# Optimization experiments

Measured on AMD Instinct MI355X. Metric: run time of the kernel, lower is better.

The kernel has to match this reference:

```python
import jax, jax.numpy as jnp
import numpy as np

BATCH = 8
N_POINTS = 2048
HOP = 1  # hop_length


def setup_inputs() -> dict:
    key = jax.random.key(0)
    kx = jax.random.fold_in(key, 0)
    x = jax.random.normal(kx, (BATCH, N_POINTS), dtype=jnp.float32)
    # learnable window-width parameter (init_lambd = 20.0)
    lambd = jnp.full((1,), 20.0, dtype=jnp.float32)
    return {"x": x, "lambd": lambd}


def reference(x, lambd):
    """Batched differentiable Gaussian-window spectrogram.

    Equivalent to looping over the batch and calling
    tf.differentiable_spectrogram(x[i] - mean(x[i]), |lambd|, hop_length=HOP):
    a Gaussian window over the WHOLE signal centered at t_c = 0, HOP, ..., n,
    followed by a zero-padded one-sided FFT (n_fft = 2n) and power spectrum.
    Output: (B, 1, n+1, n//HOP + 1).
    """
    B, n = x.shape
    sigma = jnp.abs(lambd)[0]
    # per-sample mean subtraction
    x = x - jnp.mean(x, axis=1, keepdims=True)
    t = jnp.arange(n, dtype=jnp.float32)                       # (n,)
    t_c = jnp.arange(0, n + 1, HOP, dtype=jnp.float32)         # (F,) frame centers
    # Gaussian windows over the whole signal, one per frame center: (F, n)
    windows = jnp.exp(-0.5 * jnp.square((t[None, :] - t_c[:, None]) / sigma))
    # windowed signals: (B, F, n)
    xw = x[:, None, :] * windows[None, :, :]
    # zero-padded one-sided FFT -> n+1 frequency bins: (B, F, n+1)
    spec = jnp.fft.rfft(xw, n=2 * n, axis=-1)
    power = spec.real ** 2 + spec.imag ** 2                    # power spectrogram
    # (B, 1, n+1 freq, F time)
    return jnp.swapaxes(power, 1, 2)[:, None, :, :]
```

## Files before the change

kernel.cpp:

```cpp
#include <hip/hip_runtime.h>
#include <math.h>

#define NPTS    2048
#define NBINS   2049
#define NFRAMES 2049
#define U       192
#define PAD     96
#define XPLEN   2560

#define MTOT    4224
#define MBLK    33
#define NBLK    9
#define BM      128
#define BN      256
#define BK      64
#define SPAN    (BN + U)
#define SSTRIDE 464
#define NCOPY   8
#define ASTRIDE 72
#define ABUF    (BM * ASTRIDE)

typedef __attribute__((ext_vector_type(8))) short short8_t;
typedef __attribute__((ext_vector_type(4))) float float4_t;

static __device__ __forceinline__ unsigned short f2bf(float f) {
    unsigned u = __float_as_uint(f);
    unsigned r = (u + 0x7fffu + ((u >> 16) & 1u)) >> 16;
    return (unsigned short)r;
}

#define WCH 6
#define WGBLK ((MTOT * WCH + 255) / 256)
__global__ void prep_kernel(const float* __restrict__ x, const float* __restrict__ lambd,
                            unsigned short* __restrict__ xp, unsigned short* __restrict__ W) {
    if (blockIdx.x < 8) {
        __shared__ float red[256];
        const int b = blockIdx.x;
        float s = 0.f;
        for (int t = threadIdx.x; t < NPTS; t += 256) s += x[b * NPTS + t];
        red[threadIdx.x] = s;
        __syncthreads();
        for (int off = 128; off > 0; off >>= 1) {
            if (threadIdx.x < off) red[threadIdx.x] += red[threadIdx.x + off];
            __syncthreads();
        }
        const float mean = red[0] * (1.f / (float)NPTS);
        for (int t = threadIdx.x; t < XPLEN; t += 256) {
            const int s2 = t - PAD;
            float v = (s2 >= 0 && s2 < NPTS) ? (x[b * NPTS + s2] - mean) : 0.f;
            xp[b * XPLEN + t] = f2bf(v);
        }
        return;
    }
    const int idx = (blockIdx.x - 8) * 256 + threadIdx.x;
    if (idx >= MTOT * WCH) return;
    const int m  = idx / WCH;
    const int ch = idx - m * WCH;
    const int k = m >> 1, p = m & 1;
    unsigned int* wp = (unsigned int*)(W + (size_t)m * U + ch * 32);
    if (k >= NBINS) {
        #pragma unroll
        for (int j = 0; j < 16; ++j) wp[j] = 0u;
        return;
    }
    const float sigma  = fabsf(lambd[0]);
    const float inv2s2 = 0.5f / (sigma * sigma);
    const int   u0i = ch * 32 - PAD;
    const float u0  = (float)u0i;
    const float TWO_PI = 6.28318530717958647692f;
    float sn, cs, sd, cd;
    __sincosf(TWO_PI * (1.f / 4096.f) * (float)((k * u0i) & 4095), &sn, &cs);
    __sincosf(TWO_PI * (1.f / 4096.f) * (float)k, &sd, &cd);
    float       g  = __expf(-u0 * u0 * inv2s2);
    float       gr = __expf(-(2.f * u0 + 1.f) * inv2s2);
    const float gq = __expf(-2.f * inv2s2);
    #pragma unroll
    for (int j = 0; j < 16; ++j) {
        unsigned short lo = f2bf(g * (p ? sn : cs));
        float cn = cs * cd - sn * sd; sn = fmaf(sn, cd, cs * sd); cs = cn;
        g *= gr; gr *= gq;
        unsigned short hi = f2bf(g * (p ? sn : cs));
        cn = cs * cd - sn * sd; sn = fmaf(sn, cd, cs * sd); cs = cn;
        g *= gr; gr *= gq;
        wp[j] = (unsigned int)lo | ((unsigned int)hi << 16);
    }
}

__global__ __launch_bounds__(256, 2) void spec_mfma(
        const unsigned short* __restrict__ W, const unsigned short* __restrict__ xp,
        float* __restrict__ out) {
    __shared__ unsigned short Alds[2 * ABUF];
    __shared__ unsigned short span[NCOPY * SSTRIDE];

    const int tid = threadIdx.x;
    const int b  = blockIdx.z;
    const int n0 = blockIdx.x * BN;
    const int m0 = blockIdx.y * BM;

    {
        const unsigned short* xpb = xp + b * XPLEN;
        for (int i = tid; i < NCOPY * SPAN; i += 256) {
            const int c = i / SPAN;
            const int t = i - c * SPAN;
            span[c * SSTRIDE + t] = xpb[n0 + t + c];
        }
    }

    const int lane = tid & 63;
    const int wv   = tid >> 6;
    const int wm   = (wv & 1) * 64;
    const int wn   = (wv >> 1) * 128;
    const int col  = lane & 15;
    const int q    = lane >> 4;

    const int row  = tid >> 1;
    const int half = tid & 1;
    const unsigned short* wrow = W + (size_t)(m0 + row) * U + half * 32;
    const int lbase = row * ASTRIDE + half * 32;

    const int cc = col & 7;
    const unsigned short* bbase = span + cc * SSTRIDE + (wn + col - cc) + 8 * q;

    float4_t acc[4][8];
    #pragma unroll
    for (int mt = 0; mt < 4; ++mt)
        #pragma unroll
        for (int nt = 0; nt < 8; ++nt)
            acc[mt][nt] = (float4_t){0.f, 0.f, 0.f, 0.f};

    float4 r0, r1, r2, r3;
    {
        const float4* g4 = (const float4*)(wrow);
        r0 = g4[0]; r1 = g4[1]; r2 = g4[2]; r3 = g4[3];
        float4* l4 = (float4*)(Alds + lbase);
        l4[0] = r0; l4[1] = r1; l4[2] = r2; l4[3] = r3;
        const float4* g5 = (const float4*)(wrow + BK);
        r0 = g5[0]; r1 = g5[1]; r2 = g5[2]; r3 = g5[3];
    }
    __syncthreads();

    short8_t bf[8];
    #pragma unroll
    for (int d = 0; d < 8; ++d)
        bf[d] = *(const short8_t*)(bbase + 16 * d);

    #pragma unroll
    for (int s = 0; s < 3; ++s) {
        if (s < 2) {
            float4* l4 = (float4*)(Alds + ((s + 1) & 1) * ABUF + lbase);
            l4[0] = r0; l4[1] = r1; l4[2] = r2; l4[3] = r3;
        }
        if (s < 1) {
            const float4* g4 = (const float4*)(wrow + (s + 2) * BK);
            r0 = g4[0]; r1 = g4[1]; r2 = g4[2]; r3 = g4[3];
        }
        const unsigned short* cur = Alds + (s & 1) * ABUF;
        #pragma unroll
        for (int ks = 0; ks < 2; ++ks) {
            const int j  = s * 2 + ks;
            const int kk = ks * 32;
            short8_t af[4];
            #pragma unroll
            for (int mt = 0; mt < 4; ++mt)
                af[mt] = *(const short8_t*)(cur + (wm + mt * 16 + col) * ASTRIDE + kk + q * 8);
            short8_t nb0, nb1;
            if (j < 5) {
                nb0 = *(const short8_t*)(bbase + 16 * (2 * j + 8));
                nb1 = *(const short8_t*)(bbase + 16 * (2 * j + 9));
            }
            #pragma unroll
            for (int mt = 0; mt < 4; ++mt)
                #pragma unroll
                for (int nt = 0; nt < 8; ++nt)
                    acc[mt][nt] = __builtin_amdgcn_mfma_f32_16x16x32_bf16(
                        af[mt], bf[(nt + 2 * j) & 7], acc[mt][nt], 0, 0, 0);
            if (j < 5) {
                bf[(2 * j) & 7]     = nb0;
                bf[(2 * j + 1) & 7] = nb1;
            }
        }
        __syncthreads();
    }

    const int fbase = n0 + wn + col;
    #pragma unroll
    for (int mt = 0; mt < 4; ++mt) {
        const int mrow = m0 + wm + mt * 16 + q * 4;
        const int kk0  = mrow >> 1;
        #pragma unroll
        for (int nt = 0; nt < 8; ++nt) {
            const int f = fbase + nt * 16;
            if (f < NFRAMES) {
                const float4_t a = acc[mt][nt];
                const float p0 = a[0] * a[0] + a[1] * a[1];
                const float p1 = a[2] * a[2] + a[3] * a[3];
                if (kk0 < NBINS)
                    out[((size_t)b * NBINS + kk0) * NFRAMES + f] = p0;
                if (kk0 + 1 < NBINS)
                    out[((size_t)b * NBINS + kk0 + 1) * NFRAMES + f] = p1;
            }
        }
    }
}

extern "C" void kernel_launch(void* const* d_in, const int* in_sizes, int n_in,
                              void* d_out, int out_size, void* d_ws, size_t ws_size,
                              hipStream_t stream) {
    const float* x     = (const float*)d_in[0];
    const float* lambd = (const float*)d_in[1];
    float*       out   = (float*)d_out;

    char* ws = (char*)d_ws;
    unsigned short* xp = (unsigned short*)ws;
    unsigned short* W  = (unsigned short*)(ws + 43264);

    hipLaunchKernelGGL(prep_kernel, dim3(8 + WGBLK), dim3(256), 0, stream, x, lambd, xp, W);

    dim3 grid(NBLK, MBLK, 8);
    hipLaunchKernelGGL(spec_mfma, grid, dim3(256), 0, stream, W, xp, out);
}
```

Before: 172.1 us.

## Load A operand fragments directly from global memory, drop LDS staging

The W (A-operand) tiles are now read straight from global/L2 into registers in the MFMA fragment layout, with one-step register double buffering. This replaces the LDS double-buffered staging, removing LDS writes, LDS reads and the per-stage barriers. The span fill also writes two bf16 values per 32-bit store. The trade-off is uncoalesced 16-byte global loads per lane, and two waves sharing the same rows both fetch A, so more L2 traffic and global latency now sit on the MFMA critical path.

Result: slower. 176.0 us (+2.3%).

```diff
diff --git a/kernel.cpp b/kernel.cpp
--- a/kernel.cpp
+++ b/kernel.cpp
@@ -13,12 +13,9 @@
 #define NBLK    9
 #define BM      128
 #define BN      256
-#define BK      64
 #define SPAN    (BN + U)
 #define SSTRIDE 464
 #define NCOPY   8
-#define ASTRIDE 72
-#define ABUF    (BM * ASTRIDE)
 
 typedef __attribute__((ext_vector_type(8))) short short8_t;
 typedef __attribute__((ext_vector_type(4))) float float4_t;
@@ -89,7 +86,6 @@
 __global__ __launch_bounds__(256, 2) void spec_mfma(
         const unsigned short* __restrict__ W, const unsigned short* __restrict__ xp,
         float* __restrict__ out) {
-    __shared__ unsigned short Alds[2 * ABUF];
     __shared__ unsigned short span[NCOPY * SSTRIDE];
 
     const int tid = threadIdx.x;
@@ -99,10 +95,12 @@
 
     {
         const unsigned short* xpb = xp + b * XPLEN;
-        for (int i = tid; i < NCOPY * SPAN; i += 256) {
-            const int c = i / SPAN;
-            const int t = i - c * SPAN;
-            span[c * SSTRIDE + t] = xpb[n0 + t + c];
+        for (int i = tid; i < NCOPY * (SPAN / 2); i += 256) {
+            const int c  = i / (SPAN / 2);
+            const int t2 = (i - c * (SPAN / 2)) * 2;
+            const unsigned lo = xpb[n0 + t2 + c];
+            const unsigned hi = xpb[n0 + t2 + c + 1];
+            *(unsigned*)(span + c * SSTRIDE + t2) = lo | (hi << 16);
         }
     }
 
@@ -113,10 +111,7 @@
     const int col  = lane & 15;
     const int q    = lane >> 4;
 
-    const int row  = tid >> 1;
-    const int half = tid & 1;
-    const unsigned short* wrow = W + (size_t)(m0 + row) * U + half * 32;
-    const int lbase = row * ASTRIDE + half * 32;
+    const unsigned short* abase = W + (size_t)(m0 + wm + col) * U + q * 8;
 
     const int cc = col & 7;
     const unsigned short* bbase = span + cc * SSTRIDE + (wn + col - cc) + 8 * q;
@@ -128,15 +123,11 @@
         for (int nt = 0; nt < 8; ++nt)
             acc[mt][nt] = (float4_t){0.f, 0.f, 0.f, 0.f};
 
-    float4 r0, r1, r2, r3;
-    {
-        const float4* g4 = (const float4*)(wrow);
-        r0 = g4[0]; r1 = g4[1]; r2 = g4[2]; r3 = g4[3];
-        float4* l4 = (float4*)(Alds + lbase);
-        l4[0] = r0; l4[1] = r1; l4[2] = r2; l4[3] = r3;
-        const float4* g5 = (const float4*)(wrow + BK);
-        r0 = g5[0]; r1 = g5[1]; r2 = g5[2]; r3 = g5[3];
-    }
+    short8_t afc[4], afn[4];
+    #pragma unroll
+    for (int mt = 0; mt < 4; ++mt)
+        afc[mt] = *(const short8_t*)(abase + mt * 16 * U);
+
     __syncthreads();
 
     short8_t bf[8];
@@ -145,41 +136,28 @@
         bf[d] = *(const short8_t*)(bbase + 16 * d);
 
     #pragma unroll
-    for (int s = 0; s < 3; ++s) {
-        if (s < 2) {
-            float4* l4 = (float4*)(Alds + ((s + 1) & 1) * ABUF + lbase);
-            l4[0] = r0; l4[1] = r1; l4[2] = r2; l4[3] = r3;
-        }
-        if (s < 1) {
-            const float4* g4 = (const float4*)(wrow + (s + 2) * BK);
-            r0 = g4[0]; r1 = g4[1]; r2 = g4[2]; r3 = g4[3];
-        }
-        const unsigned short* cur = Alds + (s & 1) * ABUF;
-        #pragma unroll
-        for (int ks = 0; ks < 2; ++ks) {
-            const int j  = s * 2 + ks;
-            const int kk = ks * 32;
-            short8_t af[4];
+    for (int j = 0; j < 6; ++j) {
+        short8_t nb0, nb1;
+        if (j < 5) {
             #pragma unroll
             for (int mt = 0; mt < 4; ++mt)
-                af[mt] = *(const short8_t*)(cur + (wm + mt * 16 + col) * ASTRIDE + kk + q * 8);
-            short8_t nb0, nb1;
-            if (j < 5) {
-                nb0 = *(const short8_t*)(bbase + 16 * (2 * j + 8));
-                nb1 = *(const short8_t*)(bbase + 16 * (2 * j + 9));
-            }
+                afn[mt] = *(const short8_t*)(abase + mt * 16 * U + (j + 1) * 32);
+            nb0 = *(const short8_t*)(bbase + 16 * (2 * j + 8));
+            nb1 = *(const short8_t*)(bbase + 16 * (2 * j + 9));
+        }
+        #pragma unroll
+        for (int mt = 0; mt < 4; ++mt)
+            #pragma unroll
+            for (int nt = 0; nt < 8; ++nt)
+                acc[mt][nt] = __builtin_amdgcn_mfma_f32_16x16x32_bf16(
+                    afc[mt], bf[(nt + 2 * j) & 7], acc[mt][nt], 0, 0, 0);
+        if (j < 5) {
+            bf[(2 * j) & 7]     = nb0;
+            bf[(2 * j + 1) & 7] = nb1;
             #pragma unroll
             for (int mt = 0; mt < 4; ++mt)
-                #pragma unroll
-                for (int nt = 0; nt < 8; ++nt)
-                    acc[mt][nt] = __builtin_amdgcn_mfma_f32_16x16x32_bf16(
-                        af[mt], bf[(nt + 2 * j) & 7], acc[mt][nt], 0, 0, 0);
-            if (j < 5) {
-                bf[(2 * j) & 7]     = nb0;
-                bf[(2 * j + 1) & 7] = nb1;
-            }
+                afc[mt] = afn[mt];
         }
-        __syncthreads();
     }
 
     const int fbase = n0 + wn + col;
```
